# Kernel optimization log

Hardware: AMD Instinct MI355X
Metric: run time of the kernel (lower is better)

## Reference

```python
import jax, jax.numpy as jnp
import numpy as np

GRID = 128
DIMS = [64 + 3, 128, 64, 32, 1]  # MLP channel stack from source


def setup_inputs() -> dict:
    key = jax.random.key(0)
    ks = jax.random.split(key, 1 + 2 * (len(DIMS) - 1))
    B = 1
    inp = {"x": jax.random.normal(ks[0], (B, 64, 1, 1), dtype=jnp.float32)}
    for i in range(len(DIMS) - 1):
        cin, cout = DIMS[i], DIMS[i + 1]
        scale = 1.0 / np.sqrt(cin)
        inp[f"W{i+1}"] = jax.random.uniform(ks[1 + 2 * i], (cout, cin), jnp.float32, -scale, scale)
        inp[f"b{i+1}"] = jax.random.uniform(ks[2 + 2 * i], (cout,), jnp.float32, -scale, scale)
    return inp


def _forward(x, W1, b1, W2, b2, W3, b3, W4, b4):
    B = x.shape[0]
    dt = x.dtype
    lines = jnp.linspace(-1.0, 1.0, GRID, dtype=dt)
    a, b, c = jnp.meshgrid(lines, lines, lines, indexing="ij")  # torch default 'ij'
    pts = jnp.stack([a, b, c], axis=0).reshape(3, -1)           # [3, N], N = 128^3
    N = pts.shape[1]
    # broadcast latent over all grid points and concat coords -> [B, 67, N]
    f = jnp.concatenate(
        [jnp.broadcast_to(x.reshape(B, 64, 1), (B, 64, N)),
         jnp.broadcast_to(pts[None], (B, 3, N))],
        axis=1,
    )
    h = jax.nn.relu(jnp.einsum("oc,bcn->bon", W1, f) + b1[:, None])
    h = jax.nn.relu(jnp.einsum("oc,bcn->bon", W2, h) + b2[:, None])
    h = jax.nn.relu(jnp.einsum("oc,bcn->bon", W3, h) + b3[:, None])
    sdf = jax.nn.sigmoid(jnp.einsum("oc,bcn->bon", W4, h) + b4[:, None])  # [B,1,N]
    return sdf.reshape(B, GRID, GRID, GRID)


def reference(x, W1, b1, W2, b2, W3, b3, W4, b4):
    return _forward(x, W1, b1, W2, b2, W3, b3, W4, b4)
```

## Files before the change

### kernel.cpp

```cpp
#include <hip/hip_runtime.h>
#include <hip/hip_bf16.h>
#include <hip/hip_fp16.h>


#define NPTS (128 * 128 * 128)

typedef float f32x4_t __attribute__((ext_vector_type(4)));
typedef float f32x2_t __attribute__((ext_vector_type(2)));
typedef __fp16 g16x2_t __attribute__((ext_vector_type(2)));
typedef _Float16 h16x8_t __attribute__((ext_vector_type(8)));

__device__ __forceinline__ unsigned h2u(g16x2_t h) {
    unsigned u;
    __builtin_memcpy(&u, &h, 4);
    return u;
}
__device__ __forceinline__ g16x2_t u2h(unsigned u) {
    g16x2_t h;
    __builtin_memcpy(&h, &u, 4);
    return h;
}

__global__ __launch_bounds__(256, 2) void mlp_kernel(
    const float* __restrict__ x,  const float* __restrict__ W1,
    const float* __restrict__ b1, const float* __restrict__ W2,
    const float* __restrict__ b2, const float* __restrict__ W3,
    const float* __restrict__ b3, const float* __restrict__ W4,
    const float* __restrict__ b4, float* __restrict__ out) {
    __shared__ __align__(16) unsigned s_basep[32][64];
    __shared__ __align__(16) unsigned s_wcp[64];
    __shared__ __align__(16) float s_b2[64];
    __shared__ __align__(16) float s_b3[32];
    __shared__ __align__(16) float s_w4[32];
    __shared__ __align__(16) unsigned short s_u[22528];

    const int t = threadIdx.x;
    const int w = t >> 6;
    const int lane = t & 63;
    const int quad = lane >> 4;
    const int l15 = lane & 15;
    const float step = 2.0f / 127.0f;

    {
        const int p = t & 63, h = t >> 6;
        const float* r0 = W1 + (2 * p) * 67 + h * 16;
        const float* r1 = r0 + 67;
        const float* xh = x + h * 16;
        float s0 = 0.0f, s1 = 0.0f;
#pragma unroll
        for (int c = 0; c < 16; ++c) {
            const float xc = xh[c];
            s0 = fmaf(r0[c], xc, s0);
            s1 = fmaf(r1[c], xc, s1);
        }
        float2* psum = (float2*)&s_u[10240];
        psum[h * 64 + p] = make_float2(s0, s1);
    }
    const float2* W2v = (const float2*)W2;
#pragma unroll
    for (int it = 0; it < 16; ++it) {
        int pidx = t + 256 * it;
        int idx2 = pidx * 2;
        int o = idx2 >> 7, k = idx2 & 127;
        int mt = o >> 4, lm = o & 15;
        int kb = k >> 5, q = (k >> 3) & 3, jj = k & 7;
        float2 v = W2v[pidx];
        *(unsigned*)&s_u[(mt * 4 + kb) * 512 + (q * 16 + lm) * 8 + jj] =
            h2u(__builtin_amdgcn_cvt_pkrtz(v.x, v.y));
    }
    const float2* W3v = (const float2*)W3;
#pragma unroll
    for (int it = 0; it < 4; ++it) {
        int pidx = t + 256 * it;
        int idx2 = pidx * 2;
        int o = idx2 >> 6, k = idx2 & 63;
        int mt = o >> 4, lm = o & 15;
        int kb = k >> 5, q = (k >> 3) & 3, jj = k & 7;
        float2 v = W3v[pidx];
        *(unsigned*)&s_u[8192 + (mt * 2 + kb) * 512 + (q * 16 + lm) * 8 + jj] =
            h2u(__builtin_amdgcn_cvt_pkrtz(v.x, v.y));
    }
    if (t < 64) s_b2[t] = b2[t];
    if (t < 32) {
        s_b3[t] = b3[t];
        s_w4[t] = W4[t];
    }
    const float bias4 = b4[0];
    __syncthreads();

    if (t < 64) {
        const float2* psum = (const float2*)&s_u[10240];
        float2 q0 = psum[t], q1 = psum[64 + t], q2 = psum[128 + t], q3 = psum[192 + t];
        float s0 = b1[2 * t] + (q0.x + q1.x) + (q2.x + q3.x);
        float s1 = b1[2 * t + 1] + (q0.y + q1.y) + (q2.y + q3.y);
        const float* r0 = W1 + (2 * t) * 67;
        const float* r1 = r0 + 67;
        const float pa = -1.0f + step * (float)(blockIdx.x >> 2);
        const float base0 = fmaf(r0[64], pa, s0);
        const float base1 = fmaf(r1[64], pa, s1);
        const float wb0 = r0[65], wb1 = r1[65];
        const int gj0 = (blockIdx.x & 3) * 32;
        s_wcp[t] = h2u(__builtin_amdgcn_cvt_pkrtz(r0[66], r1[66]));
#pragma unroll
        for (int j = 0; j < 32; ++j) {
            const float pb = -1.0f + step * (float)(gj0 + j);
            s_basep[j][t] = h2u(__builtin_amdgcn_cvt_pkrtz(
                fmaf(wb0, pb, base0), fmaf(wb1, pb, base1)));
        }
    }
    __syncthreads();

    h16x8_t a2[16];
#pragma unroll
    for (int f = 0; f < 16; ++f) a2[f] = *(const h16x8_t*)&s_u[f * 512 + lane * 8];
    h16x8_t a3[4];
#pragma unroll
    for (int f = 0; f < 4; ++f) a3[f] = *(const h16x8_t*)&s_u[8192 + f * 512 + lane * 8];
    f32x4_t b2q[4];
#pragma unroll
    for (int mt = 0; mt < 4; ++mt) b2q[mt] = *(const f32x4_t*)&s_b2[mt * 16 + quad * 4];
    f32x4_t b3q[2];
    f32x2_t w4lo[2], w4hi[2];
#pragma unroll
    for (int mt = 0; mt < 2; ++mt) {
        b3q[mt] = *(const f32x4_t*)&s_b3[mt * 16 + quad * 4];
        float4 wq = *(const float4*)&s_w4[mt * 16 + quad * 4];
        w4lo[mt][0] = wq.x; w4lo[mt][1] = wq.y;
        w4hi[mt][0] = wq.z; w4hi[mt][1] = wq.w;
    }
    unsigned twp[16];
#pragma unroll
    for (int kb = 0; kb < 4; ++kb) {
        uint4 v = *(const uint4*)&s_wcp[kb * 16 + quad * 4];
        twp[kb * 4 + 0] = v.x; twp[kb * 4 + 1] = v.y;
        twp[kb * 4 + 2] = v.z; twp[kb * 4 + 3] = v.w;
    }
#pragma unroll
    for (int i = 0; i < 16; ++i) asm volatile("" : "+v"(twp[i]));
    __syncthreads();

    const int sw = (l15 & 1) * 32;
    unsigned short* h2w = &s_u[w * 4608];
    float* zf = (float*)&s_u[18432];
    const f32x2_t zero2 = {0.0f, 0.0f};
    const g16x2_t zero2h = {(__fp16)0.0f, (__fp16)0.0f};
    const int outbase = blockIdx.x * 4096 + w * 1024;

    unsigned tbp[16];
    auto aphase2 = [&](int pgX, int pgY, f32x4_t accX[4], f32x4_t accY[4]) {
        const float pcX = fmaf(step, (float)((pgX * 16) + l15), -1.0f);
        const float pcY = fmaf(step, (float)((pgY * 16) + l15), -1.0f);
        const g16x2_t pc2X = __builtin_amdgcn_cvt_pkrtz(pcX, pcX);
        const g16x2_t pc2Y = __builtin_amdgcn_cvt_pkrtz(pcY, pcY);
        h16x8_t bfX[4], bfY[4];
#pragma unroll
        for (int kb = 0; kb < 4; ++kb) {
            union { h16x8_t v; g16x2_t h[4]; } bx, by;
#pragma unroll
            for (int p = 0; p < 4; ++p) {
                g16x2_t tw = u2h(twp[kb * 4 + p]);
                g16x2_t tb = u2h(tbp[kb * 4 + p]);
                g16x2_t hx = __builtin_elementwise_fma(tw, pc2X, tb);
                g16x2_t hy = __builtin_elementwise_fma(tw, pc2Y, tb);
                bx.h[p] = __builtin_elementwise_max(hx, zero2h);
                by.h[p] = __builtin_elementwise_max(hy, zero2h);
            }
            bfX[kb] = bx.v;
            bfY[kb] = by.v;
        }
#pragma unroll
        for (int mt = 0; mt < 4; ++mt) {
            f32x4_t cX = b2q[mt], cY = b2q[mt];
#pragma unroll
            for (int kb = 0; kb < 4; ++kb) {
                cX = __builtin_amdgcn_mfma_f32_16x16x32_f16(a2[mt * 4 + kb], bfX[kb], cX, 0, 0, 0);
                cY = __builtin_amdgcn_mfma_f32_16x16x32_f16(a2[mt * 4 + kb], bfY[kb], cY, 0, 0, 0);
            }
            accX[mt] = cX;
            accY[mt] = cY;
        }
    };
    auto a3store2 = [&](int ngX, int ngY, const f32x4_t accX[4], const f32x4_t accY[4]) {
        unsigned short* slotX = h2w + (ngX & 3) * 1152 + l15 * 72;
        unsigned short* slotY = h2w + (ngY & 3) * 1152 + l15 * 72;
#pragma unroll
        for (int mt = 0; mt < 4; ++mt) {
            g16x2_t loX = __builtin_elementwise_max(
                __builtin_amdgcn_cvt_pkrtz(accX[mt][0], accX[mt][1]), zero2h);
            g16x2_t loY = __builtin_elementwise_max(
                __builtin_amdgcn_cvt_pkrtz(accY[mt][0], accY[mt][1]), zero2h);
            g16x2_t hiX = __builtin_elementwise_max(
                __builtin_amdgcn_cvt_pkrtz(accX[mt][2], accX[mt][3]), zero2h);
            g16x2_t hiY = __builtin_elementwise_max(
                __builtin_amdgcn_cvt_pkrtz(accY[mt][2], accY[mt][3]), zero2h);
            uint2 pkX, pkY;
            pkX.x = h2u(loX); pkX.y = h2u(hiX);
            pkY.x = h2u(loY); pkY.y = h2u(hiY);
            *(uint2*)&slotX[(mt * 16 + quad * 4) ^ sw] = pkX;
            *(uint2*)&slotY[(mt * 16 + quad * 4) ^ sw] = pkY;
        }
    };
    auto bphase2 = [&](int pgA, h16x8_t af0, h16x8_t af1,
                       int pgB, h16x8_t bf0, h16x8_t bf1) {
        f32x2_t zA = zero2, zB = zero2;
#pragma unroll
        for (int mt = 0; mt < 2; ++mt) {
            f32x4_t cA = b3q[mt], cB = b3q[mt];
            cA = __builtin_amdgcn_mfma_f32_16x16x32_f16(a3[mt * 2 + 0], af0, cA, 0, 0, 0);
            cB = __builtin_amdgcn_mfma_f32_16x16x32_f16(a3[mt * 2 + 0], bf0, cB, 0, 0, 0);
            cA = __builtin_amdgcn_mfma_f32_16x16x32_f16(a3[mt * 2 + 1], af1, cA, 0, 0, 0);
            cB = __builtin_amdgcn_mfma_f32_16x16x32_f16(a3[mt * 2 + 1], bf1, cB, 0, 0, 0);
            f32x2_t hA01 = __builtin_elementwise_max((f32x2_t){cA[0], cA[1]}, zero2);
            f32x2_t hB01 = __builtin_elementwise_max((f32x2_t){cB[0], cB[1]}, zero2);
            f32x2_t hA23 = __builtin_elementwise_max((f32x2_t){cA[2], cA[3]}, zero2);
            f32x2_t hB23 = __builtin_elementwise_max((f32x2_t){cB[2], cB[3]}, zero2);
            zA = __builtin_elementwise_fma(w4lo[mt], hA01, zA);
            zB = __builtin_elementwise_fma(w4lo[mt], hB01, zB);
            zA = __builtin_elementwise_fma(w4hi[mt], hA23, zA);
            zB = __builtin_elementwise_fma(w4hi[mt], hB23, zB);
        }
        zf[w * 512 + (pgA & 7) * 64 + l15 * 4 + quad] = zA[0] + zA[1];
        zf[w * 512 + (pgB & 7) * 64 + l15 * 4 + quad] = zB[0] + zB[1];
    };
    auto cphase = [&](int batch) {
#pragma unroll
        for (int half = 0; half < 2; ++half) {
            const int p = lane + 64 * half;
            const int pg = p >> 4, i = p & 15;
            float4 v = *(const float4*)&zf[w * 512 + pg * 64 + i * 4];
            float z = (v.x + v.y) + (v.z + v.w) + bias4;
            out[outbase + batch * 128 + p] = 1.0f / (1.0f + __expf(-z));
        }
    };

    for (int jr = 0; jr < 8; ++jr) {
        const unsigned* bp = &s_basep[w * 8 + jr][0];
#pragma unroll
        for (int kb = 0; kb < 4; ++kb) {
            uint4 v = *(const uint4*)&bp[kb * 16 + quad * 4];
            tbp[kb * 4 + 0] = v.x; tbp[kb * 4 + 1] = v.y;
            tbp[kb * 4 + 2] = v.z; tbp[kb * 4 + 3] = v.w;
        }
#pragma unroll
        for (int i = 0; i < 16; ++i) asm volatile("" : "+v"(tbp[i]));

#pragma unroll 2
        for (int pgp = 0; pgp < 4; ++pgp) {
            const int pgX = 2 * pgp, pgY = pgX + 1;
            const int ngX = jr * 8 + pgX, ngY = ngX + 1;
            h16x8_t bxf0, bxf1, byf0, byf1;
            if (ngX > 1) {
                const unsigned short* ps0 = h2w + ((ngX - 2) & 3) * 1152 + l15 * 72;
                bxf0 = *(const h16x8_t*)&ps0[(0 ^ sw) + quad * 8];
                bxf1 = *(const h16x8_t*)&ps0[(32 ^ sw) + quad * 8];
                const unsigned short* ps1 = h2w + ((ngY - 2) & 3) * 1152 + l15 * 72;
                byf0 = *(const h16x8_t*)&ps1[(0 ^ sw) + quad * 8];
                byf1 = *(const h16x8_t*)&ps1[(32 ^ sw) + quad * 8];
            }
            f32x4_t accX[4], accY[4];
            aphase2(pgX, pgY, accX, accY);
            a3store2(ngX, ngY, accX, accY);
            if (ngX > 1) {
                bphase2(ngX - 2, bxf0, bxf1, ngY - 2, byf0, byf1);
                if (((ngY - 2) & 7) == 7) cphase((ngY - 2) >> 3);
            }
        }
    }
    {
        const unsigned short* ps0 = h2w + (62 & 3) * 1152 + l15 * 72;
        h16x8_t bxf0 = *(const h16x8_t*)&ps0[(0 ^ sw) + quad * 8];
        h16x8_t bxf1 = *(const h16x8_t*)&ps0[(32 ^ sw) + quad * 8];
        const unsigned short* ps1 = h2w + (63 & 3) * 1152 + l15 * 72;
        h16x8_t byf0 = *(const h16x8_t*)&ps1[(0 ^ sw) + quad * 8];
        h16x8_t byf1 = *(const h16x8_t*)&ps1[(32 ^ sw) + quad * 8];
        bphase2(62, bxf0, bxf1, 63, byf0, byf1);
        cphase(7);
    }
}

extern "C" void kernel_launch(void* const* d_in, const int* in_sizes, int n_in,
                              void* d_out, int out_size, void* d_ws, size_t ws_size,
                              hipStream_t stream) {
    mlp_kernel<<<NPTS / 4096, 256, 0, stream>>>(
        (const float*)d_in[0], (const float*)d_in[1], (const float*)d_in[2],
        (const float*)d_in[3], (const float*)d_in[4], (const float*)d_in[5],
        (const float*)d_in[6], (const float*)d_in[7], (const float*)d_in[8],
        (float*)d_out);
}
```

Baseline: 111.1 us.

## Software-pipeline layer-2 accumulators across iterations with delayed pack-store and fixed slots

```diff
diff --git a/kernel.cpp b/kernel.cpp
--- a/kernel.cpp
+++ b/kernel.cpp
@@ -141,15 +141,16 @@
 
     const int sw = (l15 & 1) * 32;
     unsigned short* h2w = &s_u[w * 4608];
+    unsigned short* h2p = h2w + l15 * 72;
     float* zf = (float*)&s_u[18432];
     const f32x2_t zero2 = {0.0f, 0.0f};
     const g16x2_t zero2h = {(__fp16)0.0f, (__fp16)0.0f};
     const int outbase = blockIdx.x * 4096 + w * 1024;
 
     unsigned tbp[16];
-    auto aphase2 = [&](int pgX, int pgY, f32x4_t accX[4], f32x4_t accY[4]) {
-        const float pcX = fmaf(step, (float)((pgX * 16) + l15), -1.0f);
-        const float pcY = fmaf(step, (float)((pgY * 16) + l15), -1.0f);
+    auto aphase2 = [&](int pgl, f32x4_t accX[4], f32x4_t accY[4]) {
+        const float pcX = fmaf(step, (float)((pgl * 16) + l15), -1.0f);
+        const float pcY = fmaf(step, (float)(((pgl + 1) * 16) + l15), -1.0f);
         const g16x2_t pc2X = __builtin_amdgcn_cvt_pkrtz(pcX, pcX);
         const g16x2_t pc2Y = __builtin_amdgcn_cvt_pkrtz(pcY, pcY);
         h16x8_t bfX[4], bfY[4];
@@ -180,9 +181,9 @@
             accY[mt] = cY;
         }
     };
-    auto a3store2 = [&](int ngX, int ngY, const f32x4_t accX[4], const f32x4_t accY[4]) {
-        unsigned short* slotX = h2w + (ngX & 3) * 1152 + l15 * 72;
-        unsigned short* slotY = h2w + (ngY & 3) * 1152 + l15 * 72;
+    auto packstore2 = [&](int s0, int s1, const f32x4_t accX[4], const f32x4_t accY[4]) {
+        unsigned short* slotX = h2p + s0 * 1152;
+        unsigned short* slotY = h2p + s1 * 1152;
 #pragma unroll
         for (int mt = 0; mt < 4; ++mt) {
             g16x2_t loX = __builtin_elementwise_max(
@@ -200,8 +201,17 @@
             *(uint2*)&slotY[(mt * 16 + quad * 4) ^ sw] = pkY;
         }
     };
-    auto bphase2 = [&](int pgA, h16x8_t af0, h16x8_t af1,
-                       int pgB, h16x8_t bf0, h16x8_t bf1) {
+    auto prefetch2 = [&](int s0, int s1, h16x8_t& f0, h16x8_t& f1,
+                         h16x8_t& f2, h16x8_t& f3) {
+        const unsigned short* ps0 = h2p + s0 * 1152;
+        const unsigned short* ps1 = h2p + s1 * 1152;
+        f0 = *(const h16x8_t*)&ps0[(0 ^ sw) + quad * 8];
+        f1 = *(const h16x8_t*)&ps0[(32 ^ sw) + quad * 8];
+        f2 = *(const h16x8_t*)&ps1[(0 ^ sw) + quad * 8];
+        f3 = *(const h16x8_t*)&ps1[(32 ^ sw) + quad * 8];
+    };
+    auto bphase2 = [&](int zi0, int zi1, h16x8_t af0, h16x8_t af1,
+                       h16x8_t bf0, h16x8_t bf1) {
         f32x2_t zA = zero2, zB = zero2;
 #pragma unroll
         for (int mt = 0; mt < 2; ++mt) {
@@ -219,8 +229,8 @@
             zA = __builtin_elementwise_fma(w4hi[mt], hA23, zA);
             zB = __builtin_elementwise_fma(w4hi[mt], hB23, zB);
         }
-        zf[w * 512 + (pgA & 7) * 64 + l15 * 4 + quad] = zA[0] + zA[1];
-        zf[w * 512 + (pgB & 7) * 64 + l15 * 4 + quad] = zB[0] + zB[1];
+        zf[w * 512 + zi0 * 64 + l15 * 4 + quad] = zA[0] + zA[1];
+        zf[w * 512 + zi1 * 64 + l15 * 4 + quad] = zB[0] + zB[1];
     };
     auto cphase = [&](int batch) {
 #pragma unroll
@@ -233,6 +243,8 @@
         }
     };
 
+    f32x4_t aXa[4], aYa[4], aXb[4], aYb[4];
+
     for (int jr = 0; jr < 8; ++jr) {
         const unsigned* bp = &s_basep[w * 8 + jr][0];
 #pragma unroll
@@ -244,36 +256,37 @@
 #pragma unroll
         for (int i = 0; i < 16; ++i) asm volatile("" : "+v"(tbp[i]));
 
-#pragma unroll 2
-        for (int pgp = 0; pgp < 4; ++pgp) {
-            const int pgX = 2 * pgp, pgY = pgX + 1;
-            const int ngX = jr * 8 + pgX, ngY = ngX + 1;
-            h16x8_t bxf0, bxf1, byf0, byf1;
-            if (ngX > 1) {
-                const unsigned short* ps0 = h2w + ((ngX - 2) & 3) * 1152 + l15 * 72;
-                bxf0 = *(const h16x8_t*)&ps0[(0 ^ sw) + quad * 8];
-                bxf1 = *(const h16x8_t*)&ps0[(32 ^ sw) + quad * 8];
-                const unsigned short* ps1 = h2w + ((ngY - 2) & 3) * 1152 + l15 * 72;
-                byf0 = *(const h16x8_t*)&ps1[(0 ^ sw) + quad * 8];
-                byf1 = *(const h16x8_t*)&ps1[(32 ^ sw) + quad * 8];
+#pragma unroll
+        for (int pgp2 = 0; pgp2 < 2; ++pgp2) {
+            const int iE = jr * 4 + 2 * pgp2;
+            {
+                const bool doB = (iE >= 2);
+                h16x8_t f0, f1, f2, f3;
+                if (doB) prefetch2(0, 1, f0, f1, f2, f3);
+                if (pgp2 == 1 && jr >= 1) cphase(jr - 1);
+                aphase2(4 * pgp2, aXa, aYa);
+                if (doB) bphase2(pgp2 == 0 ? 4 : 0, pgp2 == 0 ? 5 : 1,
+                                 f0, f1, f2, f3);
+                if (doB) packstore2(2, 3, aXb, aYb);
             }
-            f32x4_t accX[4], accY[4];
-            aphase2(pgX, pgY, accX, accY);
-            a3store2(ngX, ngY, accX, accY);
-            if (ngX > 1) {
-                bphase2(ngX - 2, bxf0, bxf1, ngY - 2, byf0, byf1);
-                if (((ngY - 2) & 7) == 7) cphase((ngY - 2) >> 3);
+            {
+                const bool doB = (iE + 1 >= 2);
+                h16x8_t f0, f1, f2, f3;
+                if (doB) prefetch2(2, 3, f0, f1, f2, f3);
+                aphase2(4 * pgp2 + 2, aXb, aYb);
+                if (doB) bphase2(pgp2 == 0 ? 6 : 2, pgp2 == 0 ? 7 : 3,
+                                 f0, f1, f2, f3);
+                packstore2(0, 1, aXa, aYa);
             }
         }
     }
     {
-        const unsigned short* ps0 = h2w + (62 & 3) * 1152 + l15 * 72;
-        h16x8_t bxf0 = *(const h16x8_t*)&ps0[(0 ^ sw) + quad * 8];
-        h16x8_t bxf1 = *(const h16x8_t*)&ps0[(32 ^ sw) + quad * 8];
-        const unsigned short* ps1 = h2w + (63 & 3) * 1152 + l15 * 72;
-        h16x8_t byf0 = *(const h16x8_t*)&ps1[(0 ^ sw) + quad * 8];
-        h16x8_t byf1 = *(const h16x8_t*)&ps1[(32 ^ sw) + quad * 8];
-        bphase2(62, bxf0, bxf1, 63, byf0, byf1);
+        h16x8_t f0, f1, f2, f3;
+        prefetch2(0, 1, f0, f1, f2, f3);
+        bphase2(4, 5, f0, f1, f2, f3);
+        packstore2(2, 3, aXb, aYb);
+        prefetch2(2, 3, f0, f1, f2, f3);
+        bphase2(6, 7, f0, f1, f2, f3);
         cphase(7);
     }
 }
```

After: 172.2 us. 1.55x slower.
